# Performance work log

Measured on AMD Instinct MI355X. Metric: run time of the kernel, lower is better.

## Reference

```python
import jax, jax.numpy as jnp
import numpy as np

# Dims (match init_kwargs): d_model=1024, H=16 heads, hd=64, lift=2 -> Nlift=128, top-k t=32
B, T, D = 1, 2048, 1024
H, HD, LIFT, TK = 16, 64, 2, 32
N = LIFT * HD  # 128 lifted dims per head
EPS = 1e-12


def topk_sparsify(x, k):
    """ReLU then keep only the top-k values per last-dim row (rest zeroed).
    Mathematically identical to the torch COO top-k construction: the sparse
    matrix equals the dense matrix with non-top-k entries zeroed."""
    x = jax.nn.relu(x)
    vals, idx = jax.lax.top_k(x, k)              # (..., k)
    n = x.shape[-1]
    flat_idx = idx.reshape(-1, k)
    flat_vals = vals.reshape(-1, k)
    R = flat_idx.shape[0]
    out = jnp.zeros((R, n), dtype=x.dtype)
    out = out.at[jnp.arange(R)[:, None], flat_idx].set(flat_vals)
    return out.reshape(x.shape)


def setup_inputs() -> dict:
    key = jax.random.key(0)
    ks = jax.random.split(key, 6)
    x = jax.random.normal(ks[0], (B, T, D), jnp.float32)
    W_q = jax.random.normal(ks[1], (H * N, D), jnp.float32) * 0.02
    W_k = jax.random.normal(ks[2], (H * N, D), jnp.float32) * 0.02
    W_v = jax.random.normal(ks[3], (H * HD, D), jnp.float32) * 0.02
    W_o = jax.random.normal(ks[4], (D, H * HD), jnp.float32) * 0.02
    sink = jax.random.normal(ks[5], (H, HD), jnp.float32) * 0.02
    log_beta = jnp.zeros((), jnp.float32)
    return {"x": x, "W_q": W_q, "W_k": W_k, "W_v": W_v, "W_o": W_o,
            "sink": sink, "log_beta": log_beta}


def reference(x, W_q, W_k, W_v, W_o, sink, log_beta):
    # Projections (Linear with no bias: x @ W.T)
    q = (x @ W_q.T).reshape(B, T, H, N)
    k = (x @ W_k.T).reshape(B, T, H, N)
    v = (x @ W_v.T).reshape(B, T, H, HD)

    # ReLU + top-k sparsification of lifted Q/K rows
    qs = topk_sparsify(q, TK).transpose(0, 2, 1, 3)  # (B,H,T,N)
    kk = topk_sparsify(k, TK).transpose(0, 2, 1, 3)  # (B,H,T,N)

    # A = Qs @ Ks^T per (batch, head) block; spspmm only produces same-block
    # entries, so the per-head batched matmul is the exact dense equivalent.
    A = jnp.einsum('bhin,bhjn->bhij', qs, kk)        # (B,H,T,T), all >= 0

    # Causal filter: keep j <= i
    causal = jnp.tril(jnp.ones((T, T), dtype=bool))
    A = jnp.where(causal, A, jnp.zeros((), A.dtype))

    # p=1 normalization with learned sink mass beta
    denom = A.sum(-1)                                # (B,H,T)
    beta = jnp.exp(log_beta)
    denom_ws = denom + beta
    A = A / jnp.maximum(denom_ws, EPS)[..., None]

    vh = v.transpose(0, 2, 1, 3)                     # (B,H,T,HD)
    Y = jnp.einsum('bhij,bhjd->bhid', A, vh)         # (B,H,T,HD)
    Y = Y + (beta / denom_ws)[..., None] * sink[None, :, None, :]

    Y = Y.transpose(0, 2, 1, 3).reshape(B, T, H * HD)
    return Y @ W_o.T
```

## Files before the change

kernel.cpp:

```cpp
#include <hip/hip_runtime.h>

typedef __attribute__((ext_vector_type(8))) short bf8v;
typedef __attribute__((ext_vector_type(4))) float f4v;
typedef unsigned short u16;
typedef unsigned int   u32;
#define AS1 __attribute__((address_space(1)))
#define AS3 __attribute__((address_space(3)))

__device__ inline u16 f2b(float f){
  u32 u = __builtin_bit_cast(u32, f);
  u += 0x7fffu + ((u >> 16) & 1u);
  return (u16)(u >> 16);
}

__global__ __launch_bounds__(256) void conv_all(const float* __restrict__ x,  const float* __restrict__ wq,
                                                const float* __restrict__ wk, const float* __restrict__ wv,
                                                const float* __restrict__ wo,
                                                u16* xb, u16* wqb, u16* wkb, u16* wvb, u16* wob){
  int i = blockIdx.x * 256 + threadIdx.x;
  const float* src; u16* dst; int off;
  if      (i <  524288){ src = x;  dst = xb;  off = i; }
  else if (i < 1048576){ src = wq; dst = wqb; off = i -  524288; }
  else if (i < 1572864){ src = wk; dst = wkb; off = i - 1048576; }
  else if (i < 1835008){ src = wv; dst = wvb; off = i - 1572864; }
  else                 { src = wo; dst = wob; off = i - 1835008; }
  float4 v = ((const float4*)src)[off];
  uint2 r;
  r.x = (u32)f2b(v.x) | ((u32)f2b(v.y) << 16);
  r.y = (u32)f2b(v.z) | ((u32)f2b(v.w) << 16);
  ((uint2*)dst)[off] = r;
}

__device__ __forceinline__ void gemm_core(const u16* __restrict__ A, const u16* __restrict__ B,
                                          int K, int m0, int n0, u16* lds, f4v acc[4][4]){
  const int tid = threadIdx.x;
  const int l = tid & 63, w = tid >> 6;
  const int wrow = (w >> 1) * 64, wcol = (w & 1) * 64;
  #pragma unroll
  for (int a = 0; a < 4; a++)
    #pragma unroll
    for (int b = 0; b < 4; b++) acc[a][b] = (f4v)0.0f;

  const int c0 = w * 64 + l;
  const int c1 = c0 + 256;
  const int r0 = c0 >> 2, s0e = ((c0 & 3) ^ ((r0 >> 1) & 3)) * 8;
  const int r1 = c1 >> 2, s1e = ((c1 & 3) ^ ((r1 >> 1) & 3)) * 8;

  const u16* Aroot = A + (size_t)m0 * K;
  const u16* Broot = B + (size_t)n0 * K;

  auto stage = [&](int k0, int bb){
    const u16* Ab = Aroot + k0;
    const u16* Bb = Broot + k0;
    __builtin_amdgcn_global_load_lds((const AS1 void*)(Ab + (size_t)r0 * K + s0e),
                                     (AS3 void*)(lds + bb + w * 512), 16, 0, 0);
    __builtin_amdgcn_global_load_lds((const AS1 void*)(Ab + (size_t)r1 * K + s1e),
                                     (AS3 void*)(lds + bb + 2048 + w * 512), 16, 0, 0);
    __builtin_amdgcn_global_load_lds((const AS1 void*)(Bb + (size_t)r0 * K + s0e),
                                     (AS3 void*)(lds + bb + 4096 + w * 512), 16, 0, 0);
    __builtin_amdgcn_global_load_lds((const AS1 void*)(Bb + (size_t)r1 * K + s1e),
                                     (AS3 void*)(lds + bb + 6144 + w * 512), 16, 0, 0);
  };

  const int nst = K >> 5;
  stage(0, 0);
  stage(32, 8192);
  stage(64, 16384);

  const int kb = l >> 4;
  for (int i = 0; i < nst; ++i){
    int k3 = (i + 3) << 5;
    if (k3 < K) stage(k3, ((i + 3) % 5) * 8192);
    if      (i <  nst - 3) asm volatile("s_waitcnt vmcnt(12)" ::: "memory");
    else if (i == nst - 3) asm volatile("s_waitcnt vmcnt(8)"  ::: "memory");
    else if (i == nst - 2) asm volatile("s_waitcnt vmcnt(4)"  ::: "memory");
    else                   asm volatile("s_waitcnt vmcnt(0)"  ::: "memory");
    __builtin_amdgcn_sched_barrier(0);
    __builtin_amdgcn_s_barrier();

    const u16* At = lds + (i % 5) * 8192;
    const u16* Bt = At + 4096;
    bf8v af[4], bfr[4];
    #pragma unroll
    for (int mr = 0; mr < 4; mr++){
      int row = wrow + mr * 16 + (l & 15);
      af[mr] = *(const bf8v*)(At + row * 32 + ((kb ^ ((row >> 1) & 3)) * 8));
    }
    #pragma unroll
    for (int nc = 0; nc < 4; nc++){
      int row = wcol + nc * 16 + (l & 15);
      bfr[nc] = *(const bf8v*)(Bt + row * 32 + ((kb ^ ((row >> 1) & 3)) * 8));
    }
    __builtin_amdgcn_s_setprio(1);
    #pragma unroll
    for (int mr = 0; mr < 4; mr++)
      #pragma unroll
      for (int nc = 0; nc < 4; nc++)
        acc[mr][nc] = __builtin_amdgcn_mfma_f32_16x16x32_bf16(af[mr], bfr[nc], acc[mr][nc], 0, 0, 0);
    __builtin_amdgcn_s_setprio(0);
  }
}

__global__ __launch_bounds__(256) void qkv_gemm(const u16* __restrict__ xb,
                                                const u16* __restrict__ wqb, const u16* __restrict__ wkb,
                                                const u16* __restrict__ wvb,
                                                u16* qf, u16* kf, u16* vtb){
  __shared__ u16 lds[40960];
  int b = (blockIdx.x & 7) * 80 + (blockIdx.x >> 3);
  const u16* Bp; int which;
  if (b < 256)      { Bp = wqb; which = 0; }
  else if (b < 512) { Bp = wkb; which = 1; b -= 256; }
  else              { Bp = wvb; which = 2; b -= 512; }
  int sh = (which == 2) ? 3 : 4;
  int m0 = (b >> sh) * 128, n0 = (b & ((1 << sh) - 1)) * 128;

  f4v acc[4][4];
  gemm_core(xb, Bp, 1024, m0, n0, lds, acc);

  const int l = threadIdx.x & 63, w = threadIdx.x >> 6;
  const int wrow = (w >> 1) * 64, wcol = (w & 1) * 64;
  if (which < 2){
    u16* C = which ? kf : qf;
    #pragma unroll
    for (int mr = 0; mr < 4; mr++)
      #pragma unroll
      for (int nc = 0; nc < 4; nc++)
        #pragma unroll
        for (int rr = 0; rr < 4; rr++){
          int row = m0 + wrow + mr * 16 + (l >> 4) * 4 + rr;
          int col = n0 + wcol + nc * 16 + (l & 15);
          C[(size_t)row * 2048 + col] = f2b(acc[mr][nc][rr]);
        }
  } else {
    #pragma unroll
    for (int mr = 0; mr < 4; mr++)
      #pragma unroll
      for (int nc = 0; nc < 4; nc++){
        int gcol = n0 + wcol + nc * 16 + (l & 15);
        int t0 = m0 + wrow + mr * 16 + (l >> 4) * 4;
        uint2 pk;
        pk.x = (u32)f2b(acc[mr][nc][0]) | ((u32)f2b(acc[mr][nc][1]) << 16);
        pk.y = (u32)f2b(acc[mr][nc][2]) | ((u32)f2b(acc[mr][nc][3]) << 16);
        *(uint2*)(vtb + (size_t)gcol * 2048 + t0) = pk;
      }
  }
}

__global__ __launch_bounds__(256) void o_gemm(const u16* __restrict__ yb, const u16* __restrict__ wob,
                                              float* out){
  __shared__ u16 lds[40960];
  int b = (blockIdx.x & 7) * 16 + (blockIdx.x >> 3);
  int m0 = (b >> 3) * 128, n0 = (b & 7) * 128;
  f4v acc[4][4];
  gemm_core(yb, wob, 1024, m0, n0, lds, acc);
  const int l = threadIdx.x & 63, w = threadIdx.x >> 6;
  const int wrow = (w >> 1) * 64, wcol = (w & 1) * 64;
  #pragma unroll
  for (int mr = 0; mr < 4; mr++)
    #pragma unroll
    for (int nc = 0; nc < 4; nc++)
      #pragma unroll
      for (int rr = 0; rr < 4; rr++){
        int row = m0 + wrow + mr * 16 + (l >> 4) * 4 + rr;
        int col = n0 + wcol + nc * 16 + (l & 15);
        out[(size_t)row * 1024 + col] = acc[mr][nc][rr];
      }
}

__global__ __launch_bounds__(256) void topk2(const u16* __restrict__ qf, const u16* __restrict__ kf,
                                             u16* __restrict__ qsb, u16* __restrict__ ksb){
  int w = threadIdx.x >> 6, l = threadIdx.x & 63;
  int b = blockIdx.x;
  const u16* src; u16* dst;
  if (b < 8192){ src = qf; dst = qsb; } else { src = kf; dst = ksb; b -= 8192; }
  int row = b * 4 + w;
  int t = row >> 4, h = row & 15;
  u32 pair = ((const u32*)(src + (size_t)t * 2048 + h * 128))[l];
  u32 u0 = pair & 0xFFFFu, u1 = pair >> 16;
  if (u0 & 0x8000u) u0 = 0;
  if (u1 & 0x8000u) u1 = 0;
  u32 pre = 0;
  for (int bb = 14; bb >= 0; --bb){
    u32 cand = pre | (1u << bb);
    int c = __builtin_popcountll(__ballot(u0 >= cand)) + __builtin_popcountll(__ballot(u1 >= cand));
    if (c >= 32) pre = cand;
  }
  u32 o0 = (u0 >= pre) ? u0 : 0u;
  u32 o1 = (u1 >= pre) ? u1 : 0u;
  ((u32*)(dst + ((size_t)h * 2048 + t) * 128))[l] = o0 | (o1 << 16);
}

__global__ __launch_bounds__(512) void attn3(const u16* __restrict__ qs, const u16* __restrict__ ks,
                                             const u16* __restrict__ vt, const float* __restrict__ sink,
                                             const float* __restrict__ logbeta, u16* __restrict__ yout,
                                             float* __restrict__ Yp, float* __restrict__ Dp){
  __shared__ u16 Kt[2][8192];
  __shared__ u16 Vt[2][4096];
  __shared__ u16 St[8][16 * 72];
  const int tid = threadIdx.x, l = tid & 63, w = tid >> 6;
  const int b = blockIdx.x;
  const int slot = b >> 3;
  const int h = (b & 7) + 8 * (slot / 40);
  const int u = slot % 40;
  int it, chunk, nch;
  if (u < 4)       { it = u; chunk = 0; nch = 1; }
  else if (u < 12) { it = 4 + ((u - 4) >> 1);  chunk = (u - 4) & 1;  nch = 2; }
  else if (u < 24) { it = 8 + (u - 12) / 3;    chunk = (u - 12) % 3; nch = 3; }
  else             { it = 12 + ((u - 24) >> 2); chunk = (u - 24) & 3; nch = 4; }
  const int jt0 = chunk * 8;
  const int jt1 = min(jt0 + 8, 2 * it + 2);
  const int qrow0 = it * 128 + w * 16;
  const float beta = expf(logbeta[0]);

  bf8v qfr[4];
  {
    int trow = qrow0 + (l & 15);
    const u16* qrow = qs + ((size_t)h * 2048 + trow) * 128 + (l >> 4) * 8;
    #pragma unroll
    for (int kk = 0; kk < 4; kk++) qfr[kk] = *(const bf8v*)(qrow + kk * 32);
  }

  f4v accY[4];
  #pragma unroll
  for (int c = 0; c < 4; c++) accY[c] = (f4v)0.0f;
  float dsum[4] = {0.f, 0.f, 0.f, 0.f};

  const u16* kroot = ks + (size_t)h * 2048 * 128;
  const u16* vroot = vt + (size_t)h * 64 * 2048;

  auto stage = [&](int jt, int buf){
    const u16* kbase = kroot + (size_t)jt * 64 * 128;
    #pragma unroll
    for (int i = 0; i < 2; i++){
      int g = i * 512 + tid;
      int r = g >> 4, c = g & 15;
      __builtin_amdgcn_global_load_lds((const AS1 void*)(kbase + r * 128 + (c ^ (r & 7)) * 8),
                                       (AS3 void*)(&Kt[buf][(i * 512 + w * 64) * 8]), 16, 0, 0);
    }
    {
      int d = tid >> 3, c = tid & 7;
      __builtin_amdgcn_global_load_lds((const AS1 void*)(vroot + (size_t)d * 2048 + jt * 64 + (c ^ (d & 7)) * 8),
                                       (AS3 void*)(&Vt[buf][w * 512]), 16, 0, 0);
    }
  };

  stage(jt0, 0);
  __syncthreads();
  int buf = 0;
  for (int jt = jt0; jt < jt1; ++jt){
    if (jt + 1 < jt1) stage(jt + 1, buf ^ 1);

    if (jt * 64 <= qrow0 + 15){
      f4v accS[4];
      #pragma unroll
      for (int c = 0; c < 4; c++) accS[c] = (f4v)0.0f;
      __builtin_amdgcn_s_setprio(1);
      #pragma unroll
      for (int c = 0; c < 4; c++){
        int r = c * 16 + (l & 15);
        #pragma unroll
        for (int kk = 0; kk < 4; kk++){
          int ch = kk * 4 + (l >> 4);
          bf8v kfr = *(const bf8v*)(&Kt[buf][r * 128 + ((ch ^ (r & 7)) * 8)]);
          accS[c] = __builtin_amdgcn_mfma_f32_16x16x32_bf16(qfr[kk], kfr, accS[c], 0, 0, 0);
        }
      }
      __builtin_amdgcn_s_setprio(0);
      if (jt * 64 + 63 > qrow0){
        #pragma unroll
        for (int c = 0; c < 4; c++)
          #pragma unroll
          for (int rr = 0; rr < 4; rr++){
            int i = qrow0 + (l >> 4) * 4 + rr;
            int j = jt * 64 + c * 16 + (l & 15);
            if (j > i) accS[c][rr] = 0.f;
          }
      }
      #pragma unroll
      for (int c = 0; c < 4; c++)
        #pragma unroll
        for (int rr = 0; rr < 4; rr++){
          dsum[rr] += accS[c][rr];
          St[w][((l >> 4) * 4 + rr) * 72 + c * 16 + (l & 15)] = f2b(accS[c][rr]);
        }
      __builtin_amdgcn_s_setprio(1);
      #pragma unroll
      for (int k2 = 0; k2 < 2; k2++){
        bf8v afr = *(const bf8v*)(&St[w][(l & 15) * 72 + k2 * 32 + (l >> 4) * 8]);
        #pragma unroll
        for (int c = 0; c < 4; c++){
          int d = c * 16 + (l & 15);
          int ch = k2 * 4 + (l >> 4);
          bf8v vfr = *(const bf8v*)(&Vt[buf][d * 64 + ((ch ^ (d & 7)) * 8)]);
          accY[c] = __builtin_amdgcn_mfma_f32_16x16x32_bf16(afr, vfr, accY[c], 0, 0, 0);
        }
      }
      __builtin_amdgcn_s_setprio(0);
    }
    __syncthreads();
    buf ^= 1;
  }

  #pragma unroll
  for (int rr = 0; rr < 4; rr++){
    float s = dsum[rr];
    s += __shfl_xor(s, 1, 64);
    s += __shfl_xor(s, 2, 64);
    s += __shfl_xor(s, 4, 64);
    s += __shfl_xor(s, 8, 64);
    dsum[rr] = s;
  }

  if (nch == 1){
    #pragma unroll
    for (int c = 0; c < 4; c++){
      float sv = sink[h * 64 + c * 16 + (l & 15)];
      #pragma unroll
      for (int rr = 0; rr < 4; rr++){
        float den = dsum[rr] + beta;
        float inv = 1.0f / fmaxf(den, 1e-12f);
        float y = (accY[c][rr] + beta * sv) * inv;
        int row = qrow0 + (l >> 4) * 4 + rr;
        yout[(size_t)row * 1024 + h * 64 + c * 16 + (l & 15)] = f2b(y);
      }
    }
  } else {
    float* yp = Yp + ((size_t)h * 40 + u) * 8192;
    #pragma unroll
    for (int c = 0; c < 4; c++)
      #pragma unroll
      for (int rr = 0; rr < 4; rr++){
        int rowib = w * 16 + (l >> 4) * 4 + rr;
        yp[rowib * 64 + c * 16 + (l & 15)] = accY[c][rr];
      }
    if ((l & 15) == 0){
      #pragma unroll
      for (int rr = 0; rr < 4; rr++)
        Dp[((size_t)h * 40 + u) * 128 + w * 16 + (l >> 4) * 4 + rr] = dsum[rr];
    }
  }
}

__global__ __launch_bounds__(256) void attn_reduce(const float* __restrict__ Yp, const float* __restrict__ Dp,
                                                   const float* __restrict__ sink, const float* __restrict__ logbeta,
                                                   u16* __restrict__ yout){
  int blk = blockIdx.x;
  int h = blk / 12, it = 4 + blk % 12;
  int nch = it / 4 + 1;
  int u0 = (it < 8) ? 4 + (it - 4) * 2 : (it < 12) ? 12 + (it - 8) * 3 : 24 + (it - 12) * 4;
  float beta = expf(logbeta[0]);
  __shared__ float inv_s[128];
  int t = threadIdx.x;
  if (t < 128){
    float s = 0.f;
    for (int c = 0; c < nch; c++) s += Dp[((size_t)h * 40 + u0 + c) * 128 + t];
    inv_s[t] = 1.0f / fmaxf(s + beta, 1e-12f);
  }
  __syncthreads();
  const float* base = Yp + ((size_t)h * 40 + u0) * 8192;
  #pragma unroll
  for (int e = 0; e < 32; e++){
    int idx = e * 256 + t;
    float acc = 0.f;
    for (int c = 0; c < nch; c++) acc += base[c * 8192 + idx];
    int row = idx >> 6, col = idx & 63;
    float y = (acc + beta * sink[h * 64 + col]) * inv_s[row];
    yout[(size_t)(it * 128 + row) * 1024 + h * 64 + col] = f2b(y);
  }
}

extern "C" void kernel_launch(void* const* d_in, const int* in_sizes, int n_in,
                              void* d_out, int out_size, void* d_ws, size_t ws_size,
                              hipStream_t stream){
  const float* x    = (const float*)d_in[0];
  const float* Wq   = (const float*)d_in[1];
  const float* Wk   = (const float*)d_in[2];
  const float* Wv   = (const float*)d_in[3];
  const float* Wo   = (const float*)d_in[4];
  const float* sink = (const float*)d_in[5];
  const float* logb = (const float*)d_in[6];

  char* ws = (char*)d_ws;
  u16*   xb  = (u16*)(ws + 0);
  u16*   wqb = (u16*)(ws + 4194304);
  u16*   wkb = (u16*)(ws + 8388608);
  u16*   wvb = (u16*)(ws + 12582912);
  u16*   wob = (u16*)(ws + 14680064);
  u16*   qf  = (u16*)(ws + 16777216);
  u16*   kf  = (u16*)(ws + 33554432);
  u16*   qsb = (u16*)(ws + 50331648);
  u16*   ksb = (u16*)(ws + 58720256);
  u16*   vtb = (u16*)(ws + 67108864);
  u16*   yb  = (u16*)(ws + 71303168);
  float* Yp  = (float*)(ws + 16777216);
  float* Dp  = (float*)(ws + 37748736);

  conv_all<<<8192, 256, 0, stream>>>(x, Wq, Wk, Wv, Wo, xb, wqb, wkb, wvb, wob);
  qkv_gemm<<<640, 256, 0, stream>>>(xb, wqb, wkb, wvb, qf, kf, vtb);
  topk2<<<16384, 256, 0, stream>>>(qf, kf, qsb, ksb);
  attn3<<<640, 512, 0, stream>>>(qsb, ksb, vtb, sink, logb, yb, Yp, Dp);
  attn_reduce<<<192, 256, 0, stream>>>(Yp, Dp, sink, logb, yb);
  o_gemm<<<128, 256, 0, stream>>>(yb, wob, (float*)d_out);
}
```

Measured before the change: 145.1 us.

## Narrow o_gemm tiles to 128x64, rebalance attention chunks, restructure GEMM pipeline

Templates the shared GEMM core on the number of N fragments so o_gemm can use 128x64 tiles and launch 256 blocks instead of 128, which fills more compute units on the small output projection. The attention kernel now splits each query tile's key tiles evenly across its chunks, instead of fixed 8-tile chunks with a short remainder, to balance work per block. The GEMM main loop is also restructured with a peeled epilogue and per-tile precomputed row pointers. The narrower o_gemm tiles reduce data reuse per block, and the vmcnt wait counts must match the new per-stage load counts.

```diff
diff --git a/kernel.cpp b/kernel.cpp
--- a/kernel.cpp
+++ b/kernel.cpp
@@ -31,63 +31,49 @@
   ((uint2*)dst)[off] = r;
 }
 
+template<int NFR>
 __device__ __forceinline__ void gemm_core(const u16* __restrict__ A, const u16* __restrict__ B,
-                                          int K, int m0, int n0, u16* lds, f4v acc[4][4]){
+                                          int K, int m0, int n0, u16* lds, f4v (&acc)[4][NFR]){
   const int tid = threadIdx.x;
   const int l = tid & 63, w = tid >> 6;
-  const int wrow = (w >> 1) * 64, wcol = (w & 1) * 64;
+  const int wrow = (w >> 1) * 64, wcol = (w & 1) * (NFR * 16);
+  constexpr int SB = 4096 + NFR * 1024;
   #pragma unroll
   for (int a = 0; a < 4; a++)
     #pragma unroll
-    for (int b = 0; b < 4; b++) acc[a][b] = (f4v)0.0f;
-
-  const int c0 = w * 64 + l;
-  const int c1 = c0 + 256;
-  const int r0 = c0 >> 2, s0e = ((c0 & 3) ^ ((r0 >> 1) & 3)) * 8;
-  const int r1 = c1 >> 2, s1e = ((c1 & 3) ^ ((r1 >> 1) & 3)) * 8;
-
-  const u16* Aroot = A + (size_t)m0 * K;
-  const u16* Broot = B + (size_t)n0 * K;
-
-  auto stage = [&](int k0, int bb){
-    const u16* Ab = Aroot + k0;
-    const u16* Bb = Broot + k0;
-    __builtin_amdgcn_global_load_lds((const AS1 void*)(Ab + (size_t)r0 * K + s0e),
-                                     (AS3 void*)(lds + bb + w * 512), 16, 0, 0);
-    __builtin_amdgcn_global_load_lds((const AS1 void*)(Ab + (size_t)r1 * K + s1e),
-                                     (AS3 void*)(lds + bb + 2048 + w * 512), 16, 0, 0);
-    __builtin_amdgcn_global_load_lds((const AS1 void*)(Bb + (size_t)r0 * K + s0e),
-                                     (AS3 void*)(lds + bb + 4096 + w * 512), 16, 0, 0);
-    __builtin_amdgcn_global_load_lds((const AS1 void*)(Bb + (size_t)r1 * K + s1e),
-                                     (AS3 void*)(lds + bb + 6144 + w * 512), 16, 0, 0);
+    for (int b = 0; b < NFR; b++) acc[a][b] = (f4v)0.0f;
+
+  const int c0 = tid, c1 = tid + 256;
+  const int r0 = c0 >> 2, s0 = ((c0 & 3) ^ ((r0 >> 1) & 3)) * 8;
+  const int r1 = c1 >> 2, s1 = ((c1 & 3) ^ ((r1 >> 1) & 3)) * 8;
+
+  const u16* Ar0 = A + (size_t)(m0 + r0) * K + s0;
+  const u16* Ar1 = A + (size_t)(m0 + r1) * K + s1;
+  const u16* Br0 = B + (size_t)(n0 + r0) * K + s0;
+  const u16* Br1 = B + (size_t)(n0 + r1) * K + s1;
+
+  auto stage = [&](int tile, int bi){
+    int k0 = tile << 5;
+    u16* buf = lds + bi * SB;
+    __builtin_amdgcn_global_load_lds((const AS1 void*)(Ar0 + k0), (AS3 void*)(buf + w * 512),        16, 0, 0);
+    __builtin_amdgcn_global_load_lds((const AS1 void*)(Ar1 + k0), (AS3 void*)(buf + 2048 + w * 512), 16, 0, 0);
+    __builtin_amdgcn_global_load_lds((const AS1 void*)(Br0 + k0), (AS3 void*)(buf + 4096 + w * 512), 16, 0, 0);
+    if constexpr (NFR == 4)
+      __builtin_amdgcn_global_load_lds((const AS1 void*)(Br1 + k0), (AS3 void*)(buf + 6144 + w * 512), 16, 0, 0);
   };
 
-  const int nst = K >> 5;
-  stage(0, 0);
-  stage(32, 8192);
-  stage(64, 16384);
-
   const int kb = l >> 4;
-  for (int i = 0; i < nst; ++i){
-    int k3 = (i + 3) << 5;
-    if (k3 < K) stage(k3, ((i + 3) % 5) * 8192);
-    if      (i <  nst - 3) asm volatile("s_waitcnt vmcnt(12)" ::: "memory");
-    else if (i == nst - 3) asm volatile("s_waitcnt vmcnt(8)"  ::: "memory");
-    else if (i == nst - 2) asm volatile("s_waitcnt vmcnt(4)"  ::: "memory");
-    else                   asm volatile("s_waitcnt vmcnt(0)"  ::: "memory");
-    __builtin_amdgcn_sched_barrier(0);
-    __builtin_amdgcn_s_barrier();
-
-    const u16* At = lds + (i % 5) * 8192;
+  auto compute = [&](int bi){
+    const u16* At = lds + bi * SB;
     const u16* Bt = At + 4096;
-    bf8v af[4], bfr[4];
+    bf8v af[4], bfr[NFR];
     #pragma unroll
     for (int mr = 0; mr < 4; mr++){
       int row = wrow + mr * 16 + (l & 15);
       af[mr] = *(const bf8v*)(At + row * 32 + ((kb ^ ((row >> 1) & 3)) * 8));
     }
     #pragma unroll
-    for (int nc = 0; nc < 4; nc++){
+    for (int nc = 0; nc < NFR; nc++){
       int row = wcol + nc * 16 + (l & 15);
       bfr[nc] = *(const bf8v*)(Bt + row * 32 + ((kb ^ ((row >> 1) & 3)) * 8));
     }
@@ -95,10 +81,34 @@
     #pragma unroll
     for (int mr = 0; mr < 4; mr++)
       #pragma unroll
-      for (int nc = 0; nc < 4; nc++)
+      for (int nc = 0; nc < NFR; nc++)
         acc[mr][nc] = __builtin_amdgcn_mfma_f32_16x16x32_bf16(af[mr], bfr[nc], acc[mr][nc], 0, 0, 0);
     __builtin_amdgcn_s_setprio(0);
-  }
+  };
+
+  const int nst = K >> 5;
+  stage(0, 0); stage(1, 1); stage(2, 2);
+  int cbuf = 0, sbuf = 3;
+  for (int i = 0; i < nst - 3; ++i){
+    stage(i + 3, sbuf);
+    sbuf = (sbuf == 4) ? 0 : sbuf + 1;
+    if constexpr (NFR == 4) asm volatile("s_waitcnt vmcnt(12)" ::: "memory");
+    else                    asm volatile("s_waitcnt vmcnt(9)"  ::: "memory");
+    __builtin_amdgcn_s_barrier();
+    compute(cbuf);
+    cbuf = (cbuf == 4) ? 0 : cbuf + 1;
+  }
+  if constexpr (NFR == 4) asm volatile("s_waitcnt vmcnt(8)" ::: "memory");
+  else                    asm volatile("s_waitcnt vmcnt(6)" ::: "memory");
+  __builtin_amdgcn_s_barrier();
+  compute(cbuf); cbuf = (cbuf == 4) ? 0 : cbuf + 1;
+  if constexpr (NFR == 4) asm volatile("s_waitcnt vmcnt(4)" ::: "memory");
+  else                    asm volatile("s_waitcnt vmcnt(3)" ::: "memory");
+  __builtin_amdgcn_s_barrier();
+  compute(cbuf); cbuf = (cbuf == 4) ? 0 : cbuf + 1;
+  asm volatile("s_waitcnt vmcnt(0)" ::: "memory");
+  __builtin_amdgcn_s_barrier();
+  compute(cbuf);
 }
 
 __global__ __launch_bounds__(256) void qkv_gemm(const u16* __restrict__ xb,
@@ -115,7 +125,7 @@
   int m0 = (b >> sh) * 128, n0 = (b & ((1 << sh) - 1)) * 128;
 
   f4v acc[4][4];
-  gemm_core(xb, Bp, 1024, m0, n0, lds, acc);
+  gemm_core<4>(xb, Bp, 1024, m0, n0, lds, acc);
 
   const int l = threadIdx.x & 63, w = threadIdx.x >> 6;
   const int wrow = (w >> 1) * 64, wcol = (w & 1) * 64;
@@ -148,17 +158,17 @@
 
 __global__ __launch_bounds__(256) void o_gemm(const u16* __restrict__ yb, const u16* __restrict__ wob,
                                               float* out){
-  __shared__ u16 lds[40960];
-  int b = (blockIdx.x & 7) * 16 + (blockIdx.x >> 3);
-  int m0 = (b >> 3) * 128, n0 = (b & 7) * 128;
-  f4v acc[4][4];
-  gemm_core(yb, wob, 1024, m0, n0, lds, acc);
+  __shared__ u16 lds[30720];
+  int b = (blockIdx.x & 7) * 32 + (blockIdx.x >> 3);
+  int m0 = (b >> 4) * 128, n0 = (b & 15) * 64;
+  f4v acc[4][2];
+  gemm_core<2>(yb, wob, 1024, m0, n0, lds, acc);
   const int l = threadIdx.x & 63, w = threadIdx.x >> 6;
-  const int wrow = (w >> 1) * 64, wcol = (w & 1) * 64;
+  const int wrow = (w >> 1) * 64, wcol = (w & 1) * 32;
   #pragma unroll
   for (int mr = 0; mr < 4; mr++)
     #pragma unroll
-    for (int nc = 0; nc < 4; nc++)
+    for (int nc = 0; nc < 2; nc++)
       #pragma unroll
       for (int rr = 0; rr < 4; rr++){
         int row = m0 + wrow + mr * 16 + (l >> 4) * 4 + rr;
@@ -207,8 +217,9 @@
   else if (u < 12) { it = 4 + ((u - 4) >> 1);  chunk = (u - 4) & 1;  nch = 2; }
   else if (u < 24) { it = 8 + (u - 12) / 3;    chunk = (u - 12) % 3; nch = 3; }
   else             { it = 12 + ((u - 24) >> 2); chunk = (u - 24) & 3; nch = 4; }
-  const int jt0 = chunk * 8;
-  const int jt1 = min(jt0 + 8, 2 * it + 2);
+  const int tiles = 2 * it + 2;
+  const int jt0 = (tiles * chunk) / nch;
+  const int jt1 = (tiles * (chunk + 1)) / nch;
   const int qrow0 = it * 128 + w * 16;
   const float beta = expf(logbeta[0]);
 
@@ -400,5 +411,5 @@
   topk2<<<16384, 256, 0, stream>>>(qf, kf, qsb, ksb);
   attn3<<<640, 512, 0, stream>>>(qsb, ksb, vtb, sink, logb, yb, Yp, Dp);
   attn_reduce<<<192, 256, 0, stream>>>(Yp, Dp, sink, logb, yb);
-  o_gemm<<<128, 256, 0, stream>>>(yb, wob, (float*)d_out);
-}
+  o_gemm<<<256, 256, 0, stream>>>(yb, wob, (float*)d_out);
+}
```

New measurement: 149.6 us. +3.1%, slower.
